# Optimization experiments

Measured on AMD Instinct MI355X. Metric: run time of the kernel, lower is better.

## Reference

```python
import jax, jax.numpy as jnp
import numpy as np

B, T, M, D, H, DFF = 8, 512, 64, 1024, 16, 4096
DH = D // H          # 64 head dim
ROT = DH // 2        # 32 rotary dims (int(head_dim*0.5))
ROPE_BASE = 10000.0
LN_EPS = 1e-5


def layernorm(x, g, b):
    mu = jnp.mean(x, -1, keepdims=True)
    var = jnp.mean(jnp.square(x - mu), -1, keepdims=True)
    return (x - mu) * jax.lax.rsqrt(var + LN_EPS) * g + b


def rotate_half(x):
    x1, x2 = x[..., : x.shape[-1] // 2], x[..., x.shape[-1] // 2:]
    return jnp.concatenate((-x2, x1), -1)


def setup_inputs() -> dict:
    key = jax.random.key(0)
    ks = jax.random.split(key, 8)
    s = 0.02
    return {
        "x": jax.random.normal(ks[0], (B, T, D), jnp.float32),
        "memory": jax.random.normal(ks[1], (B, M, D), jnp.float32),
        "Wq": jax.random.normal(ks[2], (D, D), jnp.float32) * s,
        "bq": jnp.zeros((D,), jnp.float32),
        "Wk": jax.random.normal(ks[3], (D, D), jnp.float32) * s,
        "bk": jnp.zeros((D,), jnp.float32),
        "Wv": jax.random.normal(ks[4], (D, D), jnp.float32) * s,
        "bv": jnp.zeros((D,), jnp.float32),
        "Wo": jax.random.normal(ks[5], (D, D), jnp.float32) * s,
        "bo": jnp.zeros((D,), jnp.float32),
        "W1": jax.random.normal(ks[6], (DFF, D), jnp.float32) * s,
        "b1": jnp.zeros((DFF,), jnp.float32),
        "W2": jax.random.normal(ks[7], (D, DFF), jnp.float32) * s,
        "b2": jnp.zeros((D,), jnp.float32),
        "g_attn": jnp.ones((D,), jnp.float32),
        "beta_attn": jnp.zeros((D,), jnp.float32),
        "g_mlp": jnp.ones((D,), jnp.float32),
        "beta_mlp": jnp.zeros((D,), jnp.float32),
    }


def reference(x, memory, Wq, bq, Wk, bk, Wv, bv, Wo, bo, W1, b1, W2, b2,
              g_attn, beta_attn, g_mlp, beta_mlp):
    L = M + T
    x_full = jnp.concatenate([memory, x], axis=1)            # (B, L, D)
    xa = layernorm(x_full, g_attn, beta_attn)

    def heads(t):  # (B, L, D) -> (B, H, L, DH)
        return t.reshape(B, L, H, DH).transpose(0, 2, 1, 3)

    q = heads(xa @ Wq.T + bq)
    k = heads(xa @ Wk.T + bk)
    v = heads(xa @ Wv.T + bv)

    # partial rotary embedding on first ROT dims
    inv_freq = 1.0 / (ROPE_BASE ** (jnp.arange(0, ROT, 2, dtype=jnp.float32) / ROT))
    freqs = jnp.arange(L, dtype=jnp.float32)[:, None] * inv_freq[None, :]  # (L, ROT/2)
    emb = jnp.concatenate((freqs, freqs), -1)                # (L, ROT)
    cos = jnp.cos(emb)[None, None]                           # (1,1,L,ROT)
    sin = jnp.sin(emb)[None, None]
    q_rot, q_pass = q[..., :ROT], q[..., ROT:]
    k_rot, k_pass = k[..., :ROT], k[..., ROT:]
    q_rot = q_rot * cos + rotate_half(q_rot) * sin
    k_rot = k_rot * cos + rotate_half(k_rot) * sin
    q = jnp.concatenate((q_rot, q_pass), -1)
    k = jnp.concatenate((k_rot, k_pass), -1)

    # prompt mask: memory rows attend memory only; target rows attend memory + causal target
    idx = jnp.arange(L)
    row, col = idx[:, None], idx[None, :]
    allowed = (col < M) | ((row >= M) & (col <= row))        # (L, L) bool

    scores = jnp.einsum('bhqd,bhkd->bhqk', q, k) / jnp.sqrt(jnp.float32(DH))
    scores = jnp.where(allowed[None, None], scores, jnp.float32(-1e30))
    attn = jax.nn.softmax(scores, axis=-1)
    o = jnp.einsum('bhqk,bhkd->bhqd', attn, v)
    o = o.transpose(0, 2, 1, 3).reshape(B, L, D)
    x_full = x_full + (o @ Wo.T + bo)

    xn = layernorm(x_full, g_mlp, beta_mlp)
    h = jnp.square(jax.nn.relu(xn @ W1.T + b1))              # ReLU^2 FFN
    x_full = x_full + (h @ W2.T + b2)
    return x_full[:, M:]
```

## Files before the change

### kernel.cpp

```cpp
#include <hip/hip_runtime.h>
#include <hip/hip_bf16.h>
#include <cmath>

using bf16 = __hip_bfloat16;
typedef __attribute__((ext_vector_type(8))) __bf16 bf16x8;
typedef __attribute__((ext_vector_type(4))) float f32x4;

struct __align__(8) bf16x4s { bf16 a, b, c, d; };

__device__ inline void gload_lds16(const void* g, void* l) {
  __builtin_amdgcn_global_load_lds(
      (__attribute__((address_space(1))) void*)g,
      (__attribute__((address_space(3))) void*)l, 16, 0, 0);
}

__device__ inline f32x4 mfma16(bf16x8 a, bf16x8 b, f32x4 c) {
  return __builtin_amdgcn_mfma_f32_16x16x32_bf16(a, b, c, 0, 0, 0);
}

#define BAR() __builtin_amdgcn_s_barrier()
#define VMC(N) asm volatile("s_waitcnt vmcnt(" #N ")" ::: "memory")
#define LGKM0() asm volatile("s_waitcnt lgkmcnt(0)" ::: "memory")

template<int MODE, int CHUNK>
__device__ __forceinline__ void gemm_body(
    const bf16* __restrict__ A, int lda, long sA,
    const bf16* __restrict__ B, int ldb, long sB,
    const float* __restrict__ bias,
    void* __restrict__ Out,
    int K, int ldo, long zstride,
    const float* __restrict__ rtab,
    bf16* __restrict__ o1, bf16* __restrict__ o2, bf16* __restrict__ o3)
{
  __shared__ bf16 lds[65536];
  const int tid = threadIdx.x, lane = tid & 63, wid = tid >> 6;
  const int wr = wid >> 2, wc = wid & 3;
  const int gx = gridDim.x;
  const int bidl = blockIdx.x + gx * blockIdx.y;
  const int xcd = bidl & 7, slot_ = bidl >> 3;
  int bx, by;
  if constexpr (CHUNK == 0) {
    const int sx = gx >> 2, sy = gridDim.y >> 1;
    bx = (xcd & 3) * sx + slot_ % sx;
    by = (xcd >> 2) * sy + slot_ / sx;
  } else {
    bx = slot_ % gx;
    by = xcd * (gridDim.y >> 3) + slot_ / gx;
  }
  const int m0 = by * 256, n0 = bx * 256;
  const int z = blockIdx.z;
  const bf16* Ab = A + (long)z * sA;
  const bf16* Bb = B + (long)z * sB;
  const int nt = K >> 6;

  f32x4 acc[8][4] = {};

  auto STAGE = [&](int par, int t, int part) {
    const bf16* src = (part < 2) ? Ab : Bb;
    const int ld = (part < 2) ? lda : ldb;
    const int rb = ((part < 2) ? m0 : n0) + (part & 1) * 128;
    const int k0 = t << 6;
    bf16* dst = &lds[(par * 4 + part) * 8192];
#pragma unroll
    for (int j = 0; j < 2; ++j) {
      int idx = j * 512 + tid;
      int row = idx >> 3;
      int ce = ((idx & 7) ^ (row & 7)) << 3;
      gload_lds16(src + (long)(rb + row) * ld + k0 + ce, dst + idx * 8);
    }
  };
  auto load_a = [&](bf16x8 (&a_)[4][2], int par, int mh) {
#pragma unroll
    for (int mf = 0; mf < 4; ++mf)
#pragma unroll
      for (int kk = 0; kk < 2; ++kk) {
        int r = mh * 64 + mf * 16 + (lane & 15);
        int cb = (kk * 64 + ((lane >> 4) << 4)) ^ ((r & 7) << 4);
        a_[mf][kk] = *(const bf16x8*)&lds[(par * 4 + wr) * 8192 + r * 64 + (cb >> 1)];
      }
  };
  auto load_b = [&](bf16x8 (&b_)[2][2], int par, int nh) {
#pragma unroll
    for (int nf = 0; nf < 2; ++nf)
#pragma unroll
      for (int kk = 0; kk < 2; ++kk) {
        int r = (wc & 1) * 64 + (nh * 2 + nf) * 16 + (lane & 15);
        int cb = (kk * 64 + ((lane >> 4) << 4)) ^ ((r & 7) << 4);
        b_[nf][kk] = *(const bf16x8*)&lds[(par * 4 + 2 + (wc >> 1)) * 8192 + r * 64 + (cb >> 1)];
      }
  };
  auto qmfma = [&](bf16x8 (&a_)[4][2], bf16x8 (&b_)[2][2], int mh, int nh) {
    __builtin_amdgcn_s_setprio(1);
#pragma unroll
    for (int kk = 0; kk < 2; ++kk)
#pragma unroll
      for (int mf = 0; mf < 4; ++mf)
#pragma unroll
        for (int nf = 0; nf < 2; ++nf)
          acc[mh * 4 + mf][nh * 2 + nf] =
              mfma16(a_[mf][kk], b_[nf][kk], acc[mh * 4 + mf][nh * 2 + nf]);
    __builtin_amdgcn_s_setprio(0);
  };

  STAGE(0, 0, 0); STAGE(0, 0, 1); STAGE(0, 0, 2); STAGE(0, 0, 3);
  STAGE(1, 1, 2); STAGE(1, 1, 0);
  VMC(4);
  BAR();

  const int half = nt >> 1;
  for (int i = 0; i < half; ++i) {
    const int u = 2 * i;
    const bool full = (i < half - 1);
    bf16x8 a[4][2], b0[2][2], b1[2][2];
    load_a(a, 0, 0); load_b(b0, 0, 0);
    STAGE(1, u + 1, 3);
    BAR();
    qmfma(a, b0, 0, 0);
    BAR();
    load_b(b1, 0, 1);
    STAGE(1, u + 1, 1);
    BAR();
    qmfma(a, b1, 0, 1);
    BAR();
    load_a(a, 0, 1);
    if (full) STAGE(0, u + 2, 2);
    BAR();
    qmfma(a, b1, 1, 1);
    BAR();
    if (full) STAGE(0, u + 2, 0);
    BAR();
    qmfma(a, b0, 1, 0);
    if (full) { VMC(4); } else { VMC(0); }
    BAR();
    load_a(a, 1, 0); load_b(b0, 1, 0);
    if (full) STAGE(0, u + 2, 3);
    BAR();
    qmfma(a, b0, 0, 0);
    BAR();
    load_b(b1, 1, 1);
    if (full) STAGE(0, u + 2, 1);
    BAR();
    qmfma(a, b1, 0, 1);
    BAR();
    load_a(a, 1, 1);
    if (full) STAGE(1, u + 3, 2);
    BAR();
    qmfma(a, b1, 1, 1);
    BAR();
    if (full) STAGE(1, u + 3, 0);
    BAR();
    qmfma(a, b0, 1, 0);
    if (full) VMC(4);
    BAR();
  }

  const int cb0 = n0 + wc * 64 + (lane & 15);
  const int rb0 = m0 + wr * 128 + ((lane >> 4) << 2);

  if constexpr (MODE == 9) {
    bf16* slot = &lds[wid * 8192];
    const int l15 = lane & 15;
    const int matq = n0 >> 10;
    const int hh = ((n0 & 1023) >> 6) + wc;
    const float b0v = bias[n0 + wc * 64 + l15];
    const float b1v = bias[n0 + wc * 64 + l15 + 16];
    const float b2v = bias[n0 + wc * 64 + l15 + 32];
    const float b3v = bias[n0 + wc * 64 + l15 + 48];
#pragma unroll
    for (int mf = 0; mf < 8; ++mf) {
#pragma unroll
      for (int j = 0; j < 4; ++j) {
        int lr = mf * 16 + ((lane >> 4) << 2) + j;
        float a0 = acc[mf][0][j] + b0v;
        float a1 = acc[mf][1][j] + b1v;
        float a2 = acc[mf][2][j] + b2v;
        float a3 = acc[mf][3][j] + b3v;
        if (matq < 2) {
          int rr = m0 + wr * 128 + lr;
          int p = rr % 576;
          float cs = rtab[p * 16 + l15];
          float sn = rtab[9216 + p * 16 + l15];
          float r0 = a0 * cs - a1 * sn;
          float r1 = a1 * cs + a0 * sn;
          a0 = r0; a1 = r1;
          if (matq == 0) {
            const float QS = 0.18033688011112043f;
            a0 *= QS; a1 *= QS; a2 *= QS; a3 *= QS;
          }
        }
        int sw = (lr & 7) << 3;
        slot[lr * 64 + ((l15) ^ sw)]      = __float2bfloat16(a0);
        slot[lr * 64 + ((l15 + 16) ^ sw)] = __float2bfloat16(a1);
        slot[lr * 64 + ((l15 + 32) ^ sw)] = __float2bfloat16(a2);
        slot[lr * 64 + ((l15 + 48) ^ sw)] = __float2bfloat16(a3);
      }
    }
    __syncthreads();
    if (matq == 2) {
#pragma unroll
      for (int it = 0; it < 16; ++it) {
        int pr0 = it * 8;
        bf16 tmp[8] __attribute__((aligned(16)));
#pragma unroll
        for (int j = 0; j < 8; ++j)
          tmp[j] = slot[(pr0 + j) * 64 + (lane ^ ((j & 7) << 3))];
        int rr = m0 + wr * 128 + pr0;
        int b_ = rr / 576, p = rr - b_ * 576;
        int zh = b_ * 16 + hh;
        *(bf16x8*)(o3 + (long)zh * 36864 + (long)lane * 576 + p) =
            *(const bf16x8*)tmp;
      }
    } else {
#pragma unroll
      for (int it = 0; it < 16; ++it) {
        int u = it * 64 + lane;
        int r_s = u >> 3, c_s = u & 7;
        int rr = m0 + wr * 128 + r_s;
        bf16x8 val = *(const bf16x8*)&slot[r_s * 64 + ((c_s ^ (r_s & 7)) << 3)];
        int b_ = rr / 576, p = rr - b_ * 576;
        int zh = b_ * 16 + hh;
        if (matq == 0) {
          if (p >= 64)
            *(bf16x8*)(o1 + ((long)zh * 512 + (p - 64)) * 64 + c_s * 8) = val;
        } else {
          *(bf16x8*)(o2 + ((long)zh * 576 + p) * 64 + c_s * 8) = val;
        }
      }
    }
  } else {
#pragma unroll
    for (int mf = 0; mf < 8; ++mf) {
#pragma unroll
      for (int nf = 0; nf < 4; ++nf) {
        int c = cb0 + nf * 16;
#pragma unroll
        for (int j = 0; j < 4; ++j) {
          int rr = rb0 + mf * 16 + j;
          float v = acc[mf][nf][j];
          if constexpr (MODE == 2) {
            float t2 = fmaxf(v + bias[c], 0.0f);
            ((bf16*)Out)[(long)rr * ldo + c] = __float2bfloat16(t2 * t2);
          } else {
            ((bf16*)Out)[(long)z * zstride + (long)rr * ldo + c] = __float2bfloat16(v);
          }
        }
      }
    }
  }
}

__global__ __launch_bounds__(512) void gemm_qkv(
    const bf16* A, const bf16* B, const float* bias, const float* rtab,
    bf16* o1, bf16* o2, bf16* o3)
{
  gemm_body<9, 0>(A, 1024, 0, B, 1024, 0, bias, nullptr, 1024, 0, 0,
                  rtab, o1, o2, o3);
}
__global__ __launch_bounds__(512) void gemm_wo(
    const bf16* A, const bf16* B, bf16* Out)
{
  gemm_body<8, 1>(A, 1024, 256, B, 1024, 256, nullptr, Out, 256, 1024,
                  4194304L, nullptr, nullptr, nullptr, nullptr);
}
__global__ __launch_bounds__(512) void gemm_w1(
    const bf16* A, const bf16* B, const float* bias, bf16* Out)
{
  gemm_body<2, 0>(A, 1024, 0, B, 1024, 0, bias, Out, 1024, 4096, 0,
                  nullptr, nullptr, nullptr, nullptr);
}
__global__ __launch_bounds__(512) void gemm_w2(
    const bf16* A, const bf16* B, bf16* Out)
{
  gemm_body<8, 1>(A, 4096, 1024, B, 4096, 1024, nullptr, Out, 1024, 1024,
                  4194304L, nullptr, nullptr, nullptr, nullptr);
}

__global__ __launch_bounds__(256) void reduce_k(
    const bf16* __restrict__ part, const float* __restrict__ bias,
    const float* __restrict__ resid, float* __restrict__ out)
{
  const int row = blockIdx.x, tid = threadIdx.x;
  const long rb = (long)row * 1024 + tid * 4;
  float a0 = 0, a1 = 0, a2 = 0, a3 = 0;
#pragma unroll
  for (int z = 0; z < 4; ++z) {
    bf16x4s t = *(const bf16x4s*)(part + (long)z * 4194304 + rb);
    a0 += __bfloat162float(t.a); a1 += __bfloat162float(t.b);
    a2 += __bfloat162float(t.c); a3 += __bfloat162float(t.d);
  }
  float4 b = ((const float4*)bias)[tid];
  float4 r = *(const float4*)(resid + rb);
  float4 o;
  o.x = a0 + b.x + r.x; o.y = a1 + b.y + r.y;
  o.z = a2 + b.z + r.z; o.w = a3 + b.w + r.w;
  *(float4*)(out + rb) = o;
}

__global__ __launch_bounds__(256) void reduce_ln(
    const bf16* __restrict__ part, const float* __restrict__ bias,
    const float* __restrict__ resid, const float* __restrict__ g,
    const float* __restrict__ beta, float* __restrict__ x2,
    bf16* __restrict__ xn)
{
  const int row = blockIdx.x, tid = threadIdx.x;
  const long rb = (long)row * 1024 + tid * 4;
  float a0 = 0, a1 = 0, a2 = 0, a3 = 0;
#pragma unroll
  for (int z = 0; z < 4; ++z) {
    bf16x4s t = *(const bf16x4s*)(part + (long)z * 4194304 + rb);
    a0 += __bfloat162float(t.a); a1 += __bfloat162float(t.b);
    a2 += __bfloat162float(t.c); a3 += __bfloat162float(t.d);
  }
  float4 bb4 = ((const float4*)bias)[tid];
  float4 rr4 = *(const float4*)(resid + rb);
  float4 v;
  v.x = a0 + bb4.x + rr4.x; v.y = a1 + bb4.y + rr4.y;
  v.z = a2 + bb4.z + rr4.z; v.w = a3 + bb4.w + rr4.w;
  *(float4*)(x2 + rb) = v;

  float s = v.x + v.y + v.z + v.w;
  float s2 = v.x * v.x + v.y * v.y + v.z * v.z + v.w * v.w;
#pragma unroll
  for (int o = 32; o; o >>= 1) {
    s += __shfl_down(s, o);
    s2 += __shfl_down(s2, o);
  }
  __shared__ float red[8];
  const int w = tid >> 6, lane = tid & 63;
  if (lane == 0) { red[w] = s; red[4 + w] = s2; }
  __syncthreads();
  float S = red[0] + red[1] + red[2] + red[3];
  float S2 = red[4] + red[5] + red[6] + red[7];
  float mu = S * (1.0f / 1024.0f);
  float rs = rsqrtf(S2 * (1.0f / 1024.0f) - mu * mu + 1e-5f);
  float4 gg = ((const float4*)g)[tid];
  float4 be = ((const float4*)beta)[tid];
  bf16x4s o4;
  o4.a = __float2bfloat16((v.x - mu) * rs * gg.x + be.x);
  o4.b = __float2bfloat16((v.y - mu) * rs * gg.y + be.y);
  o4.c = __float2bfloat16((v.z - mu) * rs * gg.z + be.z);
  o4.d = __float2bfloat16((v.w - mu) * rs * gg.w + be.w);
  *(bf16x4s*)(xn + rb) = o4;
}

__global__ __launch_bounds__(256) void flash_attn(
    const bf16* __restrict__ qh, const bf16* __restrict__ kh,
    const bf16* __restrict__ vt, bf16* __restrict__ attn)
{
  __shared__ bf16 ks[2][64 * 64];
  __shared__ bf16 vs[2][64 * 64];
  __shared__ bf16 pq[64 * 64];
  const int tid = threadIdx.x, lane = tid & 63, wv = tid >> 6;
  const int bid = blockIdx.x;
  const int xcd = bid & 7, sl = bid >> 3;
  const int zh = xcd * 16 + (sl >> 3);
  const int qt = sl & 7;
  const int b = zh >> 4, h = zh & 15;
  const int q0 = qt * 64;
  const bf16* qb = qh + (long)zh * 32768 + (long)q0 * 64;
  const bf16* kb = kh + (long)zh * 36864;
  const bf16* vb = vt + (long)zh * 36864;

#pragma unroll
  for (int i = 0; i < 2; ++i) {
    int idx = i * 256 + tid;
    int row = idx >> 3;
    int ce = ((idx & 7) ^ (row & 7)) << 3;
    gload_lds16(qb + (long)row * 64 + ce, pq + idx * 8);
  }
  auto stage_kv = [&](int bb, int j) {
#pragma unroll
    for (int it = 0; it < 2; ++it) {
      int idx = it * 256 + tid;
      int row = idx >> 3;
      int ce = ((idx & 7) ^ (row & 7)) << 3;
      gload_lds16(kb + (long)(j * 64 + row) * 64 + ce, &ks[bb][idx * 8]);
    }
#pragma unroll
    for (int it = 0; it < 2; ++it) {
      int idx = it * 256 + tid;
      int row = idx >> 3;
      int ce = ((idx & 7) ^ (row & 7)) << 3;
      gload_lds16(vb + (long)row * 576 + j * 64 + ce, &vs[bb][idx * 8]);
    }
  };
  stage_kv(0, 0);
  VMC(0);
  BAR();

  bf16x8 qf[2];
  {
    int r = wv * 16 + (lane & 15);
#pragma unroll
    for (int kk = 0; kk < 2; ++kk) {
      int c0 = kk * 32 + ((lane >> 4) << 3);
      qf[kk] = *(const bf16x8*)&pq[r * 64 + (c0 ^ ((r & 7) << 3))];
    }
  }

  f32x4 acc_o[4] = {};
  float mrun[4], lrun[4];
#pragma unroll
  for (int jj = 0; jj < 4; ++jj) { mrun[jj] = -1e30f; lrun[jj] = 0.0f; }

  const int nkv = qt + 2;
  int cur = 0;
  for (int j = 0; j < nkv; ++j) {
    if (j + 1 < nkv) stage_kv(cur ^ 1, j + 1);

    f32x4 sv[4] = {};
    __builtin_amdgcn_s_setprio(1);
#pragma unroll
    for (int kk = 0; kk < 2; ++kk) {
      bf16x8 kf[4];
      int c0 = kk * 32 + ((lane >> 4) << 3);
#pragma unroll
      for (int n = 0; n < 4; ++n) {
        int r = n * 16 + (lane & 15);
        kf[n] = *(const bf16x8*)&ks[cur][r * 64 + (c0 ^ ((r & 7) << 3))];
      }
#pragma unroll
      for (int n = 0; n < 4; ++n) sv[n] = mfma16(qf[kk], kf[n], sv[n]);
    }
    __builtin_amdgcn_s_setprio(0);

    if (j == nkv - 1) {
#pragma unroll
      for (int n = 0; n < 4; ++n) {
        int c = n * 16 + (lane & 15);
#pragma unroll
        for (int jj = 0; jj < 4; ++jj) {
          int r = wv * 16 + ((lane >> 4) << 2) + jj;
          if (c > r) sv[n][jj] = -1e30f;
        }
      }
    }
#pragma unroll
    for (int jj = 0; jj < 4; ++jj) {
      float pm = fmaxf(fmaxf(sv[0][jj], sv[1][jj]), fmaxf(sv[2][jj], sv[3][jj]));
#pragma unroll
      for (int off = 1; off < 16; off <<= 1) pm = fmaxf(pm, __shfl_xor(pm, off));
      float mnew = fmaxf(mrun[jj], pm);
      float sc = exp2f(mrun[jj] - mnew);
      mrun[jj] = mnew;
      float rs = 0.0f;
#pragma unroll
      for (int n = 0; n < 4; ++n) {
        float p = exp2f(sv[n][jj] - mnew);
        sv[n][jj] = p;
        rs += p;
      }
#pragma unroll
      for (int off = 1; off < 16; off <<= 1) rs += __shfl_xor(rs, off);
      lrun[jj] = lrun[jj] * sc + rs;
#pragma unroll
      for (int nd = 0; nd < 4; ++nd) acc_o[nd][jj] *= sc;
    }
#pragma unroll
    for (int n = 0; n < 4; ++n)
#pragma unroll
      for (int jj = 0; jj < 4; ++jj) {
        int pr = wv * 16 + ((lane >> 4) << 2) + jj;
        int pc = n * 16 + (lane & 15);
        pq[pr * 64 + (pc ^ ((pr & 7) << 3))] = __float2bfloat16(sv[n][jj]);
      }
    __builtin_amdgcn_s_setprio(1);
#pragma unroll
    for (int kk = 0; kk < 2; ++kk) {
      int c0 = kk * 32 + ((lane >> 4) << 3);
      bf16x8 pa, vf[4];
      {
        int r = wv * 16 + (lane & 15);
        pa = *(const bf16x8*)&pq[r * 64 + (c0 ^ ((r & 7) << 3))];
      }
#pragma unroll
      for (int nd = 0; nd < 4; ++nd) {
        int r = nd * 16 + (lane & 15);
        vf[nd] = *(const bf16x8*)&vs[cur][r * 64 + (c0 ^ ((r & 7) << 3))];
      }
#pragma unroll
      for (int nd = 0; nd < 4; ++nd) acc_o[nd] = mfma16(pa, vf[nd], acc_o[nd]);
    }
    __builtin_amdgcn_s_setprio(0);

    if (j + 1 < nkv) {
      LGKM0();
      VMC(0);
      BAR();
      cur ^= 1;
    }
  }
  bf16* ob = attn + ((long)b * 512 + q0) * 1024 + h * 64;
#pragma unroll
  for (int jj = 0; jj < 4; ++jj) {
    float inv = 1.0f / lrun[jj];
    int r = wv * 16 + ((lane >> 4) << 2) + jj;
#pragma unroll
    for (int nd = 0; nd < 4; ++nd)
      ob[(long)r * 1024 + nd * 16 + (lane & 15)] = __float2bfloat16(acc_o[nd][jj] * inv);
  }
}

template<bool CONCAT>
__global__ __launch_bounds__(256) void ln_kernel(
    const float* __restrict__ xin, const float* __restrict__ mem,
    const float* __restrict__ g, const float* __restrict__ beta,
    bf16* __restrict__ out)
{
  const int row = blockIdx.x;
  const float* src;
  if (CONCAT) {
    int b = row / 576, p = row % 576;
    src = (p < 64) ? (mem + ((long)b * 64 + p) * 1024)
                   : (xin + ((long)b * 512 + (p - 64)) * 1024);
  } else {
    src = xin + (long)row * 1024;
  }
  const int tid = threadIdx.x;
  float4 v = ((const float4*)src)[tid];
  float s = v.x + v.y + v.z + v.w;
  float s2 = v.x * v.x + v.y * v.y + v.z * v.z + v.w * v.w;
#pragma unroll
  for (int o = 32; o; o >>= 1) {
    s += __shfl_down(s, o);
    s2 += __shfl_down(s2, o);
  }
  __shared__ float red[8];
  const int w = tid >> 6, lane = tid & 63;
  if (lane == 0) { red[w] = s; red[4 + w] = s2; }
  __syncthreads();
  float S = red[0] + red[1] + red[2] + red[3];
  float S2 = red[4] + red[5] + red[6] + red[7];
  float mu = S * (1.0f / 1024.0f);
  float rs = rsqrtf(S2 * (1.0f / 1024.0f) - mu * mu + 1e-5f);
  float4 gg = ((const float4*)g)[tid];
  float4 bb = ((const float4*)beta)[tid];
  bf16x4s o4;
  o4.a = __float2bfloat16((v.x - mu) * rs * gg.x + bb.x);
  o4.b = __float2bfloat16((v.y - mu) * rs * gg.y + bb.y);
  o4.c = __float2bfloat16((v.z - mu) * rs * gg.z + bb.z);
  o4.d = __float2bfloat16((v.w - mu) * rs * gg.w + bb.w);
  *(bf16x4s*)(out + (long)row * 1024 + tid * 4) = o4;
}

__global__ __launch_bounds__(256) void setup_kernel(
    const float* __restrict__ wq, const float* __restrict__ wk,
    const float* __restrict__ wv, const float* __restrict__ wo,
    const float* __restrict__ w1, const float* __restrict__ w2,
    const float* __restrict__ bq, const float* __restrict__ bk,
    const float* __restrict__ bv,
    bf16* __restrict__ wout, float* __restrict__ bout,
    float* __restrict__ tab)
{
  const int blk = blockIdx.x;
  if (blk < 12288) {
    long e = ((long)blk * 256 + threadIdx.x) * 4;
    const long DD = 1048576, DF = 4194304;
    const float* src; long base;
    if (e < DD)            { src = wq; base = 0; }
    else if (e < 2 * DD)   { src = wk; base = DD; }
    else if (e < 3 * DD)   { src = wv; base = 2 * DD; }
    else if (e < 4 * DD)   { src = wo; base = 3 * DD; }
    else if (e < 4 * DD + DF) { src = w1; base = 4 * DD; }
    else                   { src = w2; base = 4 * DD + DF; }
    float4 v = *(const float4*)(src + (e - base));
    bf16x4s o4;
    o4.a = __float2bfloat16(v.x);
    o4.b = __float2bfloat16(v.y);
    o4.c = __float2bfloat16(v.z);
    o4.d = __float2bfloat16(v.w);
    *(bf16x4s*)(wout + e) = o4;
  } else if (blk < 12300) {
    int i = (blk - 12288) * 256 + threadIdx.x;
    if (i < 1024)      bout[i] = bq[i];
    else if (i < 2048) bout[i] = bk[i - 1024];
    else if (i < 3072) bout[i] = bv[i - 2048];
  } else {
    int i = (blk - 12300) * 256 + threadIdx.x;
    if (i < 9216) {
      int p = i >> 4, f = i & 15;
      float invf = expf(-(float)f * 0.5756462732485114f);
      float ang = (float)p * invf;
      tab[i] = cosf(ang);
      tab[9216 + i] = sinf(ang);
    }
  }
}

extern "C" void kernel_launch(void* const* d_in, const int* in_sizes, int n_in,
                              void* d_out, int out_size, void* d_ws, size_t ws_size,
                              hipStream_t stream)
{
  (void)in_sizes; (void)n_in; (void)out_size; (void)ws_size;
  const float* x    = (const float*)d_in[0];
  const float* mem  = (const float*)d_in[1];
  const float* Wq   = (const float*)d_in[2];
  const float* bq   = (const float*)d_in[3];
  const float* Wk   = (const float*)d_in[4];
  const float* bk   = (const float*)d_in[5];
  const float* Wv   = (const float*)d_in[6];
  const float* bv   = (const float*)d_in[7];
  const float* Wo   = (const float*)d_in[8];
  const float* bo   = (const float*)d_in[9];
  const float* W1   = (const float*)d_in[10];
  const float* b1   = (const float*)d_in[11];
  const float* W2   = (const float*)d_in[12];
  const float* b2   = (const float*)d_in[13];
  const float* g_a  = (const float*)d_in[14];
  const float* bt_a = (const float*)d_in[15];
  const float* g_m  = (const float*)d_in[16];
  const float* bt_m = (const float*)d_in[17];
  float* out = (float*)d_out;

  char* ws = (char*)d_ws;
  size_t off = 0;
  auto carve = [&](size_t bytes) -> void* {
    void* p = ws + off;
    off = (off + bytes + 255) & ~(size_t)255;
    return p;
  };
  bf16*  wB    = (bf16*)carve(12582912L * 2);
  float* bqkv  = (float*)carve(3072 * 4);
  float* rtab  = (float*)carve(9216 * 2 * 4);
  bf16*  xa    = (bf16*)carve(4608L * 1024 * 2);
  bf16*  qh    = (bf16*)carve(8L * 16 * 512 * 64 * 2);
  bf16*  kh    = (bf16*)carve(8L * 16 * 576 * 64 * 2);
  bf16*  vt    = (bf16*)carve(8L * 16 * 576 * 64 * 2);
  bf16*  attn  = (bf16*)carve(4096L * 1024 * 2);
  float* x2    = (float*)carve(4096L * 1024 * 4);
  bf16*  xn    = (bf16*)carve(4096L * 1024 * 2);
  bf16*  hbuf  = (bf16*)carve(4096L * 4096 * 2);
  bf16*  partsb= (bf16*)carve(4L * 4096 * 1024 * 2);

  setup_kernel<<<12336, 256, 0, stream>>>(Wq, Wk, Wv, Wo, W1, W2,
                                          bq, bk, bv, wB, bqkv, rtab);
  ln_kernel<true><<<4608, 256, 0, stream>>>(x, mem, g_a, bt_a, xa);

  gemm_qkv<<<dim3(12, 18, 1), 512, 0, stream>>>(xa, wB, bqkv, rtab, qh, kh, vt);

  flash_attn<<<1024, 256, 0, stream>>>(qh, kh, vt, attn);

  gemm_wo<<<dim3(4, 16, 4), 512, 0, stream>>>(attn, wB + 3145728L, partsb);
  reduce_ln<<<4096, 256, 0, stream>>>(partsb, bo, x, g_m, bt_m, x2, xn);

  gemm_w1<<<dim3(16, 16, 1), 512, 0, stream>>>(xn, wB + 4194304L, b1, hbuf);

  gemm_w2<<<dim3(4, 16, 4), 512, 0, stream>>>(hbuf, wB + 8388608L, partsb);
  reduce_k<<<4096, 256, 0, stream>>>(partsb, b2, x2, out);
}
```

Measured before the change: 209.4 us.

## Overlap weight conversion with LN and attention; store residual x2 in bf16

The Wq/Wk/Wv conversion, bias copy and rope table move into the LayerNorm kernel as extra blocks. The Wo/W1/W2 fp32-to-bf16 conversion becomes trailing blocks of the flash attention launch, so it can fill idle compute units alongside attention and one launch goes away. The intermediate residual x2 is now stored in bf16 instead of fp32, which halves its write and read traffic but loses precision in the residual path. The extra attention blocks hold the same shared memory allocation, which may limit how many can be resident at once.

```diff
diff --git a/kernel.cpp b/kernel.cpp
--- a/kernel.cpp
+++ b/kernel.cpp
@@ -277,7 +277,7 @@
 
 __global__ __launch_bounds__(256) void reduce_k(
     const bf16* __restrict__ part, const float* __restrict__ bias,
-    const float* __restrict__ resid, float* __restrict__ out)
+    const bf16* __restrict__ resid, float* __restrict__ out)
 {
   const int row = blockIdx.x, tid = threadIdx.x;
   const long rb = (long)row * 1024 + tid * 4;
@@ -289,17 +289,19 @@
     a2 += __bfloat162float(t.c); a3 += __bfloat162float(t.d);
   }
   float4 b = ((const float4*)bias)[tid];
-  float4 r = *(const float4*)(resid + rb);
+  bf16x4s r = *(const bf16x4s*)(resid + rb);
   float4 o;
-  o.x = a0 + b.x + r.x; o.y = a1 + b.y + r.y;
-  o.z = a2 + b.z + r.z; o.w = a3 + b.w + r.w;
+  o.x = a0 + b.x + __bfloat162float(r.a);
+  o.y = a1 + b.y + __bfloat162float(r.b);
+  o.z = a2 + b.z + __bfloat162float(r.c);
+  o.w = a3 + b.w + __bfloat162float(r.d);
   *(float4*)(out + rb) = o;
 }
 
 __global__ __launch_bounds__(256) void reduce_ln(
     const bf16* __restrict__ part, const float* __restrict__ bias,
     const float* __restrict__ resid, const float* __restrict__ g,
-    const float* __restrict__ beta, float* __restrict__ x2,
+    const float* __restrict__ beta, bf16* __restrict__ x2,
     bf16* __restrict__ xn)
 {
   const int row = blockIdx.x, tid = threadIdx.x;
@@ -316,7 +318,10 @@
   float4 v;
   v.x = a0 + bb4.x + rr4.x; v.y = a1 + bb4.y + rr4.y;
   v.z = a2 + bb4.z + rr4.z; v.w = a3 + bb4.w + rr4.w;
-  *(float4*)(x2 + rb) = v;
+  bf16x4s xo;
+  xo.a = __float2bfloat16(v.x); xo.b = __float2bfloat16(v.y);
+  xo.c = __float2bfloat16(v.z); xo.d = __float2bfloat16(v.w);
+  *(bf16x4s*)(x2 + rb) = xo;
 
   float s = v.x + v.y + v.z + v.w;
   float s2 = v.x * v.x + v.y * v.y + v.z * v.z + v.w * v.w;
@@ -345,13 +350,33 @@
 
 __global__ __launch_bounds__(256) void flash_attn(
     const bf16* __restrict__ qh, const bf16* __restrict__ kh,
-    const bf16* __restrict__ vt, bf16* __restrict__ attn)
+    const bf16* __restrict__ vt, bf16* __restrict__ attn,
+    const float* __restrict__ cWo, const float* __restrict__ cW1,
+    const float* __restrict__ cW2, bf16* __restrict__ wrest)
 {
   __shared__ bf16 ks[2][64 * 64];
   __shared__ bf16 vs[2][64 * 64];
   __shared__ bf16 pq[64 * 64];
   const int tid = threadIdx.x, lane = tid & 63, wv = tid >> 6;
   const int bid = blockIdx.x;
+
+  if (bid >= 1024) {
+    long e = (long)(bid - 1024) * 1024 + tid * 4;
+    const long DD = 1048576, DF = 4194304;
+    const float* src; long base;
+    if (e < DD)           { src = cWo; base = 0; }
+    else if (e < DD + DF) { src = cW1; base = DD; }
+    else                  { src = cW2; base = DD + DF; }
+    float4 v = *(const float4*)(src + (e - base));
+    bf16x4s o4;
+    o4.a = __float2bfloat16(v.x);
+    o4.b = __float2bfloat16(v.y);
+    o4.c = __float2bfloat16(v.z);
+    o4.d = __float2bfloat16(v.w);
+    *(bf16x4s*)(wrest + e) = o4;
+    return;
+  }
+
   const int xcd = bid & 7, sl = bid >> 3;
   const int zh = xcd * 16 + (sl >> 3);
   const int qt = sl & 7;
@@ -501,22 +526,54 @@
   }
 }
 
-template<bool CONCAT>
-__global__ __launch_bounds__(256) void ln_kernel(
+__global__ __launch_bounds__(256) void ln_setup(
     const float* __restrict__ xin, const float* __restrict__ mem,
     const float* __restrict__ g, const float* __restrict__ beta,
-    bf16* __restrict__ out)
-{
-  const int row = blockIdx.x;
-  const float* src;
-  if (CONCAT) {
-    int b = row / 576, p = row % 576;
-    src = (p < 64) ? (mem + ((long)b * 64 + p) * 1024)
-                   : (xin + ((long)b * 512 + (p - 64)) * 1024);
-  } else {
-    src = xin + (long)row * 1024;
-  }
-  const int tid = threadIdx.x;
+    bf16* __restrict__ xa,
+    const float* __restrict__ wq, const float* __restrict__ wk,
+    const float* __restrict__ wv,
+    const float* __restrict__ bq, const float* __restrict__ bk,
+    const float* __restrict__ bv,
+    bf16* __restrict__ wout, float* __restrict__ bout,
+    float* __restrict__ tab)
+{
+  const int blk = blockIdx.x, tid = threadIdx.x;
+  if (blk >= 4608) {
+    if (blk < 7680) {
+      long e = (long)(blk - 4608) * 1024 + tid * 4;
+      const long DD = 1048576;
+      const float* src; long base;
+      if (e < DD)          { src = wq; base = 0; }
+      else if (e < 2 * DD) { src = wk; base = DD; }
+      else                 { src = wv; base = 2 * DD; }
+      float4 v = *(const float4*)(src + (e - base));
+      bf16x4s o4;
+      o4.a = __float2bfloat16(v.x);
+      o4.b = __float2bfloat16(v.y);
+      o4.c = __float2bfloat16(v.z);
+      o4.d = __float2bfloat16(v.w);
+      *(bf16x4s*)(wout + e) = o4;
+    } else if (blk < 7692) {
+      int i = (blk - 7680) * 256 + tid;
+      if (i < 1024)      bout[i] = bq[i];
+      else if (i < 2048) bout[i] = bk[i - 1024];
+      else if (i < 3072) bout[i] = bv[i - 2048];
+    } else {
+      int i = (blk - 7692) * 256 + tid;
+      if (i < 9216) {
+        int p = i >> 4, f = i & 15;
+        float invf = expf(-(float)f * 0.5756462732485114f);
+        float ang = (float)p * invf;
+        tab[i] = cosf(ang);
+        tab[9216 + i] = sinf(ang);
+      }
+    }
+    return;
+  }
+  const int row = blk;
+  int b = row / 576, p = row % 576;
+  const float* src = (p < 64) ? (mem + ((long)b * 64 + p) * 1024)
+                              : (xin + ((long)b * 512 + (p - 64)) * 1024);
   float4 v = ((const float4*)src)[tid];
   float s = v.x + v.y + v.z + v.w;
   float s2 = v.x * v.x + v.y * v.y + v.z * v.z + v.w * v.w;
@@ -540,51 +597,7 @@
   o4.b = __float2bfloat16((v.y - mu) * rs * gg.y + bb.y);
   o4.c = __float2bfloat16((v.z - mu) * rs * gg.z + bb.z);
   o4.d = __float2bfloat16((v.w - mu) * rs * gg.w + bb.w);
-  *(bf16x4s*)(out + (long)row * 1024 + tid * 4) = o4;
-}
-
-__global__ __launch_bounds__(256) void setup_kernel(
-    const float* __restrict__ wq, const float* __restrict__ wk,
-    const float* __restrict__ wv, const float* __restrict__ wo,
-    const float* __restrict__ w1, const float* __restrict__ w2,
-    const float* __restrict__ bq, const float* __restrict__ bk,
-    const float* __restrict__ bv,
-    bf16* __restrict__ wout, float* __restrict__ bout,
-    float* __restrict__ tab)
-{
-  const int blk = blockIdx.x;
-  if (blk < 12288) {
-    long e = ((long)blk * 256 + threadIdx.x) * 4;
-    const long DD = 1048576, DF = 4194304;
-    const float* src; long base;
-    if (e < DD)            { src = wq; base = 0; }
-    else if (e < 2 * DD)   { src = wk; base = DD; }
-    else if (e < 3 * DD)   { src = wv; base = 2 * DD; }
-    else if (e < 4 * DD)   { src = wo; base = 3 * DD; }
-    else if (e < 4 * DD + DF) { src = w1; base = 4 * DD; }
-    else                   { src = w2; base = 4 * DD + DF; }
-    float4 v = *(const float4*)(src + (e - base));
-    bf16x4s o4;
-    o4.a = __float2bfloat16(v.x);
-    o4.b = __float2bfloat16(v.y);
-    o4.c = __float2bfloat16(v.z);
-    o4.d = __float2bfloat16(v.w);
-    *(bf16x4s*)(wout + e) = o4;
-  } else if (blk < 12300) {
-    int i = (blk - 12288) * 256 + threadIdx.x;
-    if (i < 1024)      bout[i] = bq[i];
-    else if (i < 2048) bout[i] = bk[i - 1024];
-    else if (i < 3072) bout[i] = bv[i - 2048];
-  } else {
-    int i = (blk - 12300) * 256 + threadIdx.x;
-    if (i < 9216) {
-      int p = i >> 4, f = i & 15;
-      float invf = expf(-(float)f * 0.5756462732485114f);
-      float ang = (float)p * invf;
-      tab[i] = cosf(ang);
-      tab[9216 + i] = sinf(ang);
-    }
-  }
+  *(bf16x4s*)(xa + (long)row * 1024 + tid * 4) = o4;
 }
 
 extern "C" void kernel_launch(void* const* d_in, const int* in_sizes, int n_in,
@@ -627,18 +640,18 @@
   bf16*  kh    = (bf16*)carve(8L * 16 * 576 * 64 * 2);
   bf16*  vt    = (bf16*)carve(8L * 16 * 576 * 64 * 2);
   bf16*  attn  = (bf16*)carve(4096L * 1024 * 2);
-  float* x2    = (float*)carve(4096L * 1024 * 4);
+  bf16*  x2    = (bf16*)carve(4096L * 1024 * 2);
   bf16*  xn    = (bf16*)carve(4096L * 1024 * 2);
   bf16*  hbuf  = (bf16*)carve(4096L * 4096 * 2);
   bf16*  partsb= (bf16*)carve(4L * 4096 * 1024 * 2);
 
-  setup_kernel<<<12336, 256, 0, stream>>>(Wq, Wk, Wv, Wo, W1, W2,
-                                          bq, bk, bv, wB, bqkv, rtab);
-  ln_kernel<true><<<4608, 256, 0, stream>>>(x, mem, g_a, bt_a, xa);
+  ln_setup<<<7728, 256, 0, stream>>>(x, mem, g_a, bt_a, xa,
+                                     Wq, Wk, Wv, bq, bk, bv, wB, bqkv, rtab);
 
   gemm_qkv<<<dim3(12, 18, 1), 512, 0, stream>>>(xa, wB, bqkv, rtab, qh, kh, vt);
 
-  flash_attn<<<1024, 256, 0, stream>>>(qh, kh, vt, attn);
+  flash_attn<<<10240, 256, 0, stream>>>(qh, kh, vt, attn,
+                                        Wo, W1, W2, wB + 3145728L);
 
   gemm_wo<<<dim3(4, 16, 4), 512, 0, stream>>>(attn, wB + 3145728L, partsb);
   reduce_ln<<<4096, 256, 0, stream>>>(partsb, bo, x, g_m, bt_m, x2, xn);
```

After: 196.2 us, median of 3. 6.3% less time.
